# Performance work log

Measured on AMD Instinct MI355X. Metric: run time of the kernel, lower is better.

## Reference

```python
import jax, jax.numpy as jnp
import numpy as np

B, S, N, C, OUT = 16, 1024, 4096, 768, 256


def setup_inputs() -> dict:
    key = jax.random.key(0)
    k0, k1, k2, k3, k4 = jax.random.split(key, 5)
    seed_xyz = jax.random.normal(k0, (B, S, 3), jnp.float32)   # normalized seed coords
    p_last = jax.random.normal(k1, (B, N, 3), jnp.float32)     # lift3d last-stage coords
    f_last = jax.random.normal(k2, (B, C, N), jnp.float32)     # lift3d last-stage features (channel-first)
    W = jax.random.normal(k3, (OUT, C), jnp.float32) * 0.02    # Conv1d(C, 256, kernel_size=1) weight
    b = jax.random.normal(k4, (OUT,), jnp.float32) * 0.02      # Conv1d bias
    return {"seed_xyz": seed_xyz, "p_last": p_last, "f_last": f_last, "W": W, "b": b}


def reference(seed_xyz, p_last, f_last, W, b):
    # Squared pairwise distances [B,S,N] (argmin invariant to sqrt)
    d2 = (jnp.sum(seed_xyz * seed_xyz, axis=-1, keepdims=True)          # [B,S,1]
          - 2.0 * jnp.einsum('bsd,bnd->bsn', seed_xyz, p_last)          # [B,S,N]
          + jnp.sum(p_last * p_last, axis=-1)[:, None, :])              # [B,1,N]
    idx = jnp.argmin(d2, axis=-1)                                       # [B,S]
    # Gather nearest-neighbor features: [B,C,N] -> [B,C,S]
    gathered = jnp.take_along_axis(f_last, idx[:, None, :], axis=2)
    # 1x1 Conv1d projector: [B,C,S] x [OUT,C] -> [B,OUT,S]
    seed_features = jnp.einsum('bcs,oc->bos', gathered, W) + b[None, :, None]
    return seed_features
```

## Files before the change

kernel.cpp:

```cpp
#include <hip/hip_runtime.h>
#include <stdint.h>

#define B_   16
#define S_   1024
#define N_   4096
#define C_   768
#define OUT_ 256

typedef short bf16x8 __attribute__((ext_vector_type(8)));
typedef short bf16x4 __attribute__((ext_vector_type(4)));
typedef float f32x4  __attribute__((ext_vector_type(4)));

__device__ __forceinline__ unsigned short f2bf(float f) {
    unsigned int u = __float_as_uint(f);
    u += 0x7fffu + ((u >> 16) & 1u);
    return (unsigned short)(u >> 16);
}

__global__ __launch_bounds__(256) void k_wconv(const float* __restrict__ W,
                                               unsigned short* __restrict__ Wb) {
    int i = blockIdx.x * 256 + threadIdx.x;
    Wb[i] = f2bf(W[i]);
}

__global__ __launch_bounds__(256) void k_argmin(const float* __restrict__ seed,
                                                const float* __restrict__ pl,
                                                int* __restrict__ idx_out) {
    const int t    = threadIdx.x;
    const int lane = t & 63;
    const int w    = t >> 6;
    const int gw   = blockIdx.x * 4 + w;
    const int b    = gw >> 8;
    const int s0   = (gw & 255) * 4;

    float sx[4], sy[4], sz[4], s2[4], best[4];
    int   bidx[4];
#pragma unroll
    for (int j = 0; j < 4; ++j) {
        const float* sp = seed + (size_t)(b * S_ + s0 + j) * 3;
        sx[j] = sp[0]; sy[j] = sp[1]; sz[j] = sp[2];
        s2[j] = __fadd_rn(__fadd_rn(__fmul_rn(sx[j], sx[j]),
                                    __fmul_rn(sy[j], sy[j])),
                          __fmul_rn(sz[j], sz[j]));
        best[j] = 3.4e38f;
        bidx[j] = 0;
    }
    const float* pb = pl + (size_t)b * N_ * 3;

    for (int k = 0; k < N_ / 64; ++k) {
        const int   n  = k * 64 + lane;
        const float px = pb[n * 3 + 0];
        const float py = pb[n * 3 + 1];
        const float pz = pb[n * 3 + 2];
        const float p2 = __fadd_rn(__fadd_rn(__fmul_rn(px, px),
                                             __fmul_rn(py, py)),
                                   __fmul_rn(pz, pz));
#pragma unroll
        for (int j = 0; j < 4; ++j) {
            float dot = __fadd_rn(__fadd_rn(__fmul_rn(sx[j], px),
                                            __fmul_rn(sy[j], py)),
                                  __fmul_rn(sz[j], pz));
            float d2  = __fadd_rn(__fsub_rn(s2[j], __fmul_rn(2.0f, dot)), p2);
            if (d2 < best[j]) { best[j] = d2; bidx[j] = n; }
        }
    }

#pragma unroll
    for (int j = 0; j < 4; ++j) {
#pragma unroll
        for (int off = 32; off >= 1; off >>= 1) {
            float ob = __shfl_xor(best[j], off, 64);
            int   oi = __shfl_xor(bidx[j], off, 64);
            bool take = (ob < best[j]) || (ob == best[j] && oi < bidx[j]);
            if (take) { best[j] = ob; bidx[j] = oi; }
        }
        if (lane == 0) idx_out[b * S_ + s0 + j] = bidx[j];
    }
}

__global__ __launch_bounds__(256, 2) void k_pgemm(const float* __restrict__ f,
                                                  const unsigned short* __restrict__ Wb,
                                                  unsigned short* __restrict__ P) {
    __shared__ unsigned short ldsF[2][128 * 36];
    __shared__ unsigned short ldsW[2][256 * 40];
    const int t    = threadIdx.x;
    const int b    = blockIdx.x >> 5;
    const int nt   = blockIdx.x & 31;
    const int n0   = nt * 128;
    const int lane = t & 63;
    const int w    = t >> 6;
    const int wm   = w & 1;
    const int wo   = w >> 1;
    const int quad = lane >> 4, l16 = lane & 15;

    f32x4 acc[4][8];
#pragma unroll
    for (int i = 0; i < 4; ++i)
#pragma unroll
        for (int j = 0; j < 8; ++j) acc[i][j] = (f32x4){0.f, 0.f, 0.f, 0.f};

    const int cb = t >> 5;
    const int nb = t & 31;
    const float* fB = f + (size_t)b * C_ * N_ + n0 + nb * 4;
    const int wr = t >> 2;
    const int wc = t & 3;
    const unsigned short* wSrc = Wb + (size_t)wr * C_ + wc * 8;

    f32x4  v[4];
    bf16x8 wv[4];

#pragma unroll
    for (int j = 0; j < 4; ++j)
        v[j] = *(const f32x4*)(fB + (size_t)(cb * 4 + j) * N_);
#pragma unroll
    for (int i = 0; i < 4; ++i)
        wv[i] = *(const bf16x8*)(wSrc + (size_t)i * 64 * C_);
#pragma unroll
    for (int i = 0; i < 4; ++i) {
        bf16x4 pk = {(short)f2bf(v[0][i]), (short)f2bf(v[1][i]),
                     (short)f2bf(v[2][i]), (short)f2bf(v[3][i])};
        *(bf16x4*)(&ldsF[0][(nb * 4 + i) * 36 + cb * 4]) = pk;
    }
#pragma unroll
    for (int i = 0; i < 4; ++i)
        *(bf16x8*)(&ldsW[0][(wr + i * 64) * 40 + wc * 8]) = wv[i];
    __syncthreads();

#pragma unroll 2
    for (int kt = 0; kt < C_ / 32; ++kt) {
        const int rb = kt & 1;
        const unsigned short* fR = &ldsF[rb][0];
        const unsigned short* wR = &ldsW[rb][0];
        unsigned short* fW = &ldsF[rb ^ 1][0];
        unsigned short* wW = &ldsW[rb ^ 1][0];

        if (kt < C_ / 32 - 1) {
            const int k1 = (kt + 1) * 32;
#pragma unroll
            for (int j = 0; j < 4; ++j)
                v[j] = *(const f32x4*)(fB + (size_t)(k1 + cb * 4 + j) * N_);
#pragma unroll
            for (int i = 0; i < 4; ++i)
                wv[i] = *(const bf16x8*)(wSrc + (size_t)i * 64 * C_ + k1);
        }

        bf16x8 aF[4], bF[8];
#pragma unroll
        for (int mi = 0; mi < 4; ++mi) {
            const unsigned short* p = fR + (wm * 64 + mi * 16 + l16) * 36 + quad * 8;
            bf16x4 lo = *(const bf16x4*)p;
            bf16x4 hi = *(const bf16x4*)(p + 4);
            aF[mi] = __builtin_shufflevector(lo, hi, 0, 1, 2, 3, 4, 5, 6, 7);
        }
#pragma unroll
        for (int oi = 0; oi < 8; ++oi)
            bF[oi] = *(const bf16x8*)(wR + (wo * 128 + oi * 16 + l16) * 40 + quad * 8);
#pragma unroll
        for (int mi = 0; mi < 4; ++mi)
#pragma unroll
            for (int oi = 0; oi < 8; ++oi)
                acc[mi][oi] = __builtin_amdgcn_mfma_f32_16x16x32_bf16(
                    aF[mi], bF[oi], acc[mi][oi], 0, 0, 0);

        if (kt < C_ / 32 - 1) {
#pragma unroll
            for (int i = 0; i < 4; ++i) {
                bf16x4 pk = {(short)f2bf(v[0][i]), (short)f2bf(v[1][i]),
                             (short)f2bf(v[2][i]), (short)f2bf(v[3][i])};
                *(bf16x4*)(fW + (nb * 4 + i) * 36 + cb * 4) = pk;
            }
#pragma unroll
            for (int i = 0; i < 4; ++i)
                *(bf16x8*)(wW + (wr + i * 64) * 40 + wc * 8) = wv[i];
        }
        __syncthreads();
    }

    unsigned short* Pb = P + ((size_t)b * N_ + n0) * OUT_;
#pragma unroll
    for (int mi = 0; mi < 4; ++mi) {
#pragma unroll
        for (int r = 0; r < 4; ++r) {
            const int n = wm * 64 + mi * 16 + quad * 4 + r;
            unsigned short* row = Pb + (size_t)n * OUT_;
#pragma unroll
            for (int oi = 0; oi < 8; ++oi) {
                const int o = wo * 128 + oi * 16 + l16;
                row[o] = f2bf(acc[mi][oi][r]);
            }
        }
    }
}

__global__ __launch_bounds__(256) void k_out(const unsigned short* __restrict__ P,
                                             const int* __restrict__ idx,
                                             const float* __restrict__ bias,
                                             float* __restrict__ out) {
    __shared__ unsigned short tl[64 * 260];
    const int t  = threadIdx.x;
    const int b  = blockIdx.x >> 4;
    const int st = blockIdx.x & 15;
    const int s0 = st * 64;
    const unsigned short* Pb = P + (size_t)b * N_ * OUT_;

#pragma unroll
    for (int i = 0; i < 8; ++i) {
        const int g = i * 256 + t;
        const int s = g >> 5;
        const int p = g & 31;
        const int n = idx[b * S_ + s0 + s];
        const unsigned short* src = Pb + (size_t)n * OUT_ + p * 8;
        uint2 u0 = *(const uint2*)src;
        uint2 u1 = *(const uint2*)(src + 4);
        *(uint2*)(tl + s * 260 + p * 8)     = u0;
        *(uint2*)(tl + s * 260 + p * 8 + 4) = u1;
    }
    __syncthreads();

    const int lane = t & 63;
    const int w    = t >> 6;
    float* ob = out + (size_t)b * OUT_ * S_ + s0;
#pragma unroll 4
    for (int oo = 0; oo < 64; ++oo) {
        const int o = w * 64 + oo;
        const unsigned short u = tl[lane * 260 + o];
        const float val = __uint_as_float(((unsigned int)u) << 16) + bias[o];
        ob[(size_t)o * S_ + lane] = val;
    }
}

extern "C" void kernel_launch(void* const* d_in, const int* in_sizes, int n_in,
                              void* d_out, int out_size, void* d_ws, size_t ws_size,
                              hipStream_t stream) {
    const float* seed = (const float*)d_in[0];
    const float* pl   = (const float*)d_in[1];
    const float* f    = (const float*)d_in[2];
    const float* W    = (const float*)d_in[3];
    const float* bias = (const float*)d_in[4];
    float* out = (float*)d_out;

    int* idx            = (int*)d_ws;
    unsigned short* Wb  = (unsigned short*)((char*)d_ws + 65536);
    unsigned short* P   = (unsigned short*)((char*)d_ws + 524288);

    k_wconv <<<768,  256, 0, stream>>>(W, Wb);
    k_argmin<<<1024, 256, 0, stream>>>(seed, pl, idx);
    k_pgemm <<<512,  256, 0, stream>>>(f, Wb, P);
    k_out   <<<256,  256, 0, stream>>>(P, idx, bias, out);
}
```

Baseline: 328.6 us.

## Fuse argmin and projection GEMM into one interleaved launch with deeper prefetch

Merges the nearest-neighbor argmin kernel and the projection GEMM into one launch. One block in three runs a GEMM tile and the other two run argmin, so the compute-bound distance search can overlap the memory-bound feature streaming. The GEMM now prefetches feature rows two k-steps ahead with a double register buffer and uses explicit waitcnt and barrier intrinsics. The weight conversion kernel is also vectorized to eight elements per thread. The risks are higher register pressure in the merged kernel, which could lower occupancy, and load imbalance between the two block types.

```diff
diff --git a/kernel.cpp b/kernel.cpp
--- a/kernel.cpp
+++ b/kernel.cpp
@@ -6,6 +6,7 @@
 #define N_   4096
 #define C_   768
 #define OUT_ 256
+#define NT_  (C_ / 32)
 
 typedef short bf16x8 __attribute__((ext_vector_type(8)));
 typedef short bf16x4 __attribute__((ext_vector_type(4)));
@@ -19,175 +20,191 @@
 
 __global__ __launch_bounds__(256) void k_wconv(const float* __restrict__ W,
                                                unsigned short* __restrict__ Wb) {
-    int i = blockIdx.x * 256 + threadIdx.x;
-    Wb[i] = f2bf(W[i]);
-}
-
-__global__ __launch_bounds__(256) void k_argmin(const float* __restrict__ seed,
-                                                const float* __restrict__ pl,
-                                                int* __restrict__ idx_out) {
-    const int t    = threadIdx.x;
-    const int lane = t & 63;
-    const int w    = t >> 6;
-    const int gw   = blockIdx.x * 4 + w;
-    const int b    = gw >> 8;
-    const int s0   = (gw & 255) * 4;
-
-    float sx[4], sy[4], sz[4], s2[4], best[4];
-    int   bidx[4];
-#pragma unroll
-    for (int j = 0; j < 4; ++j) {
-        const float* sp = seed + (size_t)(b * S_ + s0 + j) * 3;
-        sx[j] = sp[0]; sy[j] = sp[1]; sz[j] = sp[2];
-        s2[j] = __fadd_rn(__fadd_rn(__fmul_rn(sx[j], sx[j]),
-                                    __fmul_rn(sy[j], sy[j])),
-                          __fmul_rn(sz[j], sz[j]));
-        best[j] = 3.4e38f;
-        bidx[j] = 0;
-    }
-    const float* pb = pl + (size_t)b * N_ * 3;
-
-    for (int k = 0; k < N_ / 64; ++k) {
-        const int   n  = k * 64 + lane;
-        const float px = pb[n * 3 + 0];
-        const float py = pb[n * 3 + 1];
-        const float pz = pb[n * 3 + 2];
-        const float p2 = __fadd_rn(__fadd_rn(__fmul_rn(px, px),
-                                             __fmul_rn(py, py)),
-                                   __fmul_rn(pz, pz));
-#pragma unroll
-        for (int j = 0; j < 4; ++j) {
-            float dot = __fadd_rn(__fadd_rn(__fmul_rn(sx[j], px),
-                                            __fmul_rn(sy[j], py)),
-                                  __fmul_rn(sz[j], pz));
-            float d2  = __fadd_rn(__fsub_rn(s2[j], __fmul_rn(2.0f, dot)), p2);
-            if (d2 < best[j]) { best[j] = d2; bidx[j] = n; }
-        }
-    }
-
-#pragma unroll
-    for (int j = 0; j < 4; ++j) {
-#pragma unroll
-        for (int off = 32; off >= 1; off >>= 1) {
-            float ob = __shfl_xor(best[j], off, 64);
-            int   oi = __shfl_xor(bidx[j], off, 64);
-            bool take = (ob < best[j]) || (ob == best[j] && oi < bidx[j]);
-            if (take) { best[j] = ob; bidx[j] = oi; }
-        }
-        if (lane == 0) idx_out[b * S_ + s0 + j] = bidx[j];
-    }
-}
-
-__global__ __launch_bounds__(256, 2) void k_pgemm(const float* __restrict__ f,
+    int i = (blockIdx.x * 256 + threadIdx.x) * 8;
+    f32x4 a = *(const f32x4*)(W + i);
+    f32x4 c = *(const f32x4*)(W + i + 4);
+    bf16x8 o = {(short)f2bf(a[0]), (short)f2bf(a[1]),
+                (short)f2bf(a[2]), (short)f2bf(a[3]),
+                (short)f2bf(c[0]), (short)f2bf(c[1]),
+                (short)f2bf(c[2]), (short)f2bf(c[3])};
+    *(bf16x8*)(Wb + i) = o;
+}
+
+__global__ __launch_bounds__(256, 2) void k_fused(const float* __restrict__ f,
                                                   const unsigned short* __restrict__ Wb,
-                                                  unsigned short* __restrict__ P) {
+                                                  unsigned short* __restrict__ P,
+                                                  const float* __restrict__ seed,
+                                                  const float* __restrict__ pl,
+                                                  int* __restrict__ idx_out) {
     __shared__ unsigned short ldsF[2][128 * 36];
     __shared__ unsigned short ldsW[2][256 * 40];
-    const int t    = threadIdx.x;
-    const int b    = blockIdx.x >> 5;
-    const int nt   = blockIdx.x & 31;
-    const int n0   = nt * 128;
-    const int lane = t & 63;
-    const int w    = t >> 6;
-    const int wm   = w & 1;
-    const int wo   = w >> 1;
-    const int quad = lane >> 4, l16 = lane & 15;
-
-    f32x4 acc[4][8];
-#pragma unroll
-    for (int i = 0; i < 4; ++i)
-#pragma unroll
-        for (int j = 0; j < 8; ++j) acc[i][j] = (f32x4){0.f, 0.f, 0.f, 0.f};
-
-    const int cb = t >> 5;
-    const int nb = t & 31;
-    const float* fB = f + (size_t)b * C_ * N_ + n0 + nb * 4;
-    const int wr = t >> 2;
-    const int wc = t & 3;
-    const unsigned short* wSrc = Wb + (size_t)wr * C_ + wc * 8;
-
-    f32x4  v[4];
-    bf16x8 wv[4];
-
-#pragma unroll
-    for (int j = 0; j < 4; ++j)
-        v[j] = *(const f32x4*)(fB + (size_t)(cb * 4 + j) * N_);
-#pragma unroll
-    for (int i = 0; i < 4; ++i)
-        wv[i] = *(const bf16x8*)(wSrc + (size_t)i * 64 * C_);
-#pragma unroll
-    for (int i = 0; i < 4; ++i) {
-        bf16x4 pk = {(short)f2bf(v[0][i]), (short)f2bf(v[1][i]),
-                     (short)f2bf(v[2][i]), (short)f2bf(v[3][i])};
-        *(bf16x4*)(&ldsF[0][(nb * 4 + i) * 36 + cb * 4]) = pk;
-    }
-#pragma unroll
-    for (int i = 0; i < 4; ++i)
-        *(bf16x8*)(&ldsW[0][(wr + i * 64) * 40 + wc * 8]) = wv[i];
-    __syncthreads();
+    const int bid = blockIdx.x;
+    const int t   = threadIdx.x;
+
+    if (bid % 3 == 0) {
+        const int sub  = bid / 3;
+        const int b    = sub >> 5;
+        const int nt   = sub & 31;
+        const int n0   = nt * 128;
+        const int lane = t & 63;
+        const int w    = t >> 6;
+        const int wm   = w & 1;
+        const int wo   = w >> 1;
+        const int quad = lane >> 4, l16 = lane & 15;
+
+        f32x4 acc[4][8];
+#pragma unroll
+        for (int i = 0; i < 4; ++i)
+#pragma unroll
+            for (int j = 0; j < 8; ++j) acc[i][j] = (f32x4){0.f, 0.f, 0.f, 0.f};
+
+        const int cb = t >> 5;
+        const int nb = t & 31;
+        const float* fB = f + (size_t)b * C_ * N_ + n0 + nb * 4;
+        const int wr = t >> 2;
+        const int wc = t & 3;
+        const unsigned short* wSrc = Wb + (size_t)wr * C_ + wc * 8;
+
+        f32x4  v[2][4];
+        bf16x8 wv[4];
+
+#pragma unroll
+        for (int j = 0; j < 4; ++j)
+            v[0][j] = *(const f32x4*)(fB + (size_t)(cb * 4 + j) * N_);
+#pragma unroll
+        for (int i = 0; i < 4; ++i)
+            wv[i] = *(const bf16x8*)(wSrc + (size_t)i * 64 * C_);
+#pragma unroll
+        for (int i = 0; i < 4; ++i) {
+            bf16x4 pk = {(short)f2bf(v[0][0][i]), (short)f2bf(v[0][1][i]),
+                         (short)f2bf(v[0][2][i]), (short)f2bf(v[0][3][i])};
+            *(bf16x4*)(&ldsF[0][(nb * 4 + i) * 36 + cb * 4]) = pk;
+        }
+#pragma unroll
+        for (int i = 0; i < 4; ++i)
+            *(bf16x8*)(&ldsW[0][(wr + i * 64) * 40 + wc * 8]) = wv[i];
+#pragma unroll
+        for (int j = 0; j < 4; ++j)
+            v[1][j] = *(const f32x4*)(fB + (size_t)(32 + cb * 4 + j) * N_);
+        asm volatile("s_waitcnt lgkmcnt(0)" ::: "memory");
+        __builtin_amdgcn_sched_barrier(0);
+        __builtin_amdgcn_s_barrier();
 
 #pragma unroll 2
-    for (int kt = 0; kt < C_ / 32; ++kt) {
-        const int rb = kt & 1;
-        const unsigned short* fR = &ldsF[rb][0];
-        const unsigned short* wR = &ldsW[rb][0];
-        unsigned short* fW = &ldsF[rb ^ 1][0];
-        unsigned short* wW = &ldsW[rb ^ 1][0];
-
-        if (kt < C_ / 32 - 1) {
-            const int k1 = (kt + 1) * 32;
-#pragma unroll
-            for (int j = 0; j < 4; ++j)
-                v[j] = *(const f32x4*)(fB + (size_t)(k1 + cb * 4 + j) * N_);
-#pragma unroll
-            for (int i = 0; i < 4; ++i)
-                wv[i] = *(const bf16x8*)(wSrc + (size_t)i * 64 * C_ + k1);
-        }
-
-        bf16x8 aF[4], bF[8];
+        for (int kt = 0; kt < NT_; ++kt) {
+            const int rb = kt & 1;
+            if (kt < NT_ - 2) {
+                const int k2 = (kt + 2) * 32;
+#pragma unroll
+                for (int j = 0; j < 4; ++j)
+                    v[rb][j] = *(const f32x4*)(fB + (size_t)(k2 + cb * 4 + j) * N_);
+            }
+            if (kt < NT_ - 1) {
+                const int k1 = (kt + 1) * 32;
+#pragma unroll
+                for (int i = 0; i < 4; ++i)
+                    wv[i] = *(const bf16x8*)(wSrc + (size_t)i * 64 * C_ + k1);
+            }
+
+            bf16x8 aF[4];
+#pragma unroll
+            for (int mi = 0; mi < 4; ++mi) {
+                const unsigned short* p =
+                    &ldsF[rb][(wm * 64 + mi * 16 + l16) * 36 + quad * 8];
+                bf16x4 lo = *(const bf16x4*)p;
+                bf16x4 hi = *(const bf16x4*)(p + 4);
+                aF[mi] = __builtin_shufflevector(lo, hi, 0, 1, 2, 3, 4, 5, 6, 7);
+            }
+#pragma unroll
+            for (int oi = 0; oi < 8; ++oi) {
+                bf16x8 bF = *(const bf16x8*)(
+                    &ldsW[rb][(wo * 128 + oi * 16 + l16) * 40 + quad * 8]);
+#pragma unroll
+                for (int mi = 0; mi < 4; ++mi)
+                    acc[mi][oi] = __builtin_amdgcn_mfma_f32_16x16x32_bf16(
+                        aF[mi], bF, acc[mi][oi], 0, 0, 0);
+            }
+
+            if (kt < NT_ - 1) {
+#pragma unroll
+                for (int i = 0; i < 4; ++i) {
+                    bf16x4 pk = {(short)f2bf(v[rb ^ 1][0][i]), (short)f2bf(v[rb ^ 1][1][i]),
+                                 (short)f2bf(v[rb ^ 1][2][i]), (short)f2bf(v[rb ^ 1][3][i])};
+                    *(bf16x4*)(&ldsF[rb ^ 1][(nb * 4 + i) * 36 + cb * 4]) = pk;
+                }
+#pragma unroll
+                for (int i = 0; i < 4; ++i)
+                    *(bf16x8*)(&ldsW[rb ^ 1][(wr + i * 64) * 40 + wc * 8]) = wv[i];
+            }
+            asm volatile("s_waitcnt lgkmcnt(0)" ::: "memory");
+            __builtin_amdgcn_sched_barrier(0);
+            __builtin_amdgcn_s_barrier();
+        }
+
+        unsigned short* Pb = P + ((size_t)b * N_ + n0) * OUT_;
 #pragma unroll
         for (int mi = 0; mi < 4; ++mi) {
-            const unsigned short* p = fR + (wm * 64 + mi * 16 + l16) * 36 + quad * 8;
-            bf16x4 lo = *(const bf16x4*)p;
-            bf16x4 hi = *(const bf16x4*)(p + 4);
-            aF[mi] = __builtin_shufflevector(lo, hi, 0, 1, 2, 3, 4, 5, 6, 7);
-        }
-#pragma unroll
-        for (int oi = 0; oi < 8; ++oi)
-            bF[oi] = *(const bf16x8*)(wR + (wo * 128 + oi * 16 + l16) * 40 + quad * 8);
-#pragma unroll
-        for (int mi = 0; mi < 4; ++mi)
-#pragma unroll
-            for (int oi = 0; oi < 8; ++oi)
-                acc[mi][oi] = __builtin_amdgcn_mfma_f32_16x16x32_bf16(
-                    aF[mi], bF[oi], acc[mi][oi], 0, 0, 0);
-
-        if (kt < C_ / 32 - 1) {
-#pragma unroll
-            for (int i = 0; i < 4; ++i) {
-                bf16x4 pk = {(short)f2bf(v[0][i]), (short)f2bf(v[1][i]),
-                             (short)f2bf(v[2][i]), (short)f2bf(v[3][i])};
-                *(bf16x4*)(fW + (nb * 4 + i) * 36 + cb * 4) = pk;
-            }
-#pragma unroll
-            for (int i = 0; i < 4; ++i)
-                *(bf16x8*)(wW + (wr + i * 64) * 40 + wc * 8) = wv[i];
-        }
-        __syncthreads();
-    }
-
-    unsigned short* Pb = P + ((size_t)b * N_ + n0) * OUT_;
-#pragma unroll
-    for (int mi = 0; mi < 4; ++mi) {
-#pragma unroll
-        for (int r = 0; r < 4; ++r) {
-            const int n = wm * 64 + mi * 16 + quad * 4 + r;
-            unsigned short* row = Pb + (size_t)n * OUT_;
-#pragma unroll
-            for (int oi = 0; oi < 8; ++oi) {
-                const int o = wo * 128 + oi * 16 + l16;
-                row[o] = f2bf(acc[mi][oi][r]);
-            }
+#pragma unroll
+            for (int r = 0; r < 4; ++r) {
+                const int n = wm * 64 + mi * 16 + quad * 4 + r;
+                unsigned short* row = Pb + (size_t)n * OUT_;
+#pragma unroll
+                for (int oi = 0; oi < 8; ++oi) {
+                    const int o = wo * 128 + oi * 16 + l16;
+                    row[o] = f2bf(acc[mi][oi][r]);
+                }
+            }
+        }
+    } else {
+        const int sub  = bid - bid / 3 - 1;
+        const int lane = t & 63;
+        const int w    = t >> 6;
+        const int gw   = sub * 4 + w;
+        const int b    = gw >> 8;
+        const int s0   = (gw & 255) * 4;
+
+        float sx[4], sy[4], sz[4], s2[4], best[4];
+        int   bidx[4];
+#pragma unroll
+        for (int j = 0; j < 4; ++j) {
+            const float* sp = seed + (size_t)(b * S_ + s0 + j) * 3;
+            sx[j] = sp[0]; sy[j] = sp[1]; sz[j] = sp[2];
+            s2[j] = __fadd_rn(__fadd_rn(__fmul_rn(sx[j], sx[j]),
+                                        __fmul_rn(sy[j], sy[j])),
+                              __fmul_rn(sz[j], sz[j]));
+            best[j] = 3.4e38f;
+            bidx[j] = 0;
+        }
+        const float* pb = pl + (size_t)b * N_ * 3;
+
+        for (int k = 0; k < N_ / 64; ++k) {
+            const int   n  = k * 64 + lane;
+            const float px = pb[n * 3 + 0];
+            const float py = pb[n * 3 + 1];
+            const float pz = pb[n * 3 + 2];
+            const float p2 = __fadd_rn(__fadd_rn(__fmul_rn(px, px),
+                                                 __fmul_rn(py, py)),
+                                       __fmul_rn(pz, pz));
+#pragma unroll
+            for (int j = 0; j < 4; ++j) {
+                float dot = __fadd_rn(__fadd_rn(__fmul_rn(sx[j], px),
+                                                __fmul_rn(sy[j], py)),
+                                      __fmul_rn(sz[j], pz));
+                float d2  = __fadd_rn(__fsub_rn(s2[j], __fmul_rn(2.0f, dot)), p2);
+                if (d2 < best[j]) { best[j] = d2; bidx[j] = n; }
+            }
+        }
+
+#pragma unroll
+        for (int j = 0; j < 4; ++j) {
+#pragma unroll
+            for (int off = 32; off >= 1; off >>= 1) {
+                float ob = __shfl_xor(best[j], off, 64);
+                int   oi = __shfl_xor(bidx[j], off, 64);
+                bool take = (ob < best[j]) || (ob == best[j] && oi < bidx[j]);
+                if (take) { best[j] = ob; bidx[j] = oi; }
+            }
+            if (lane == 0) idx_out[b * S_ + s0 + j] = bidx[j];
         }
     }
 }
@@ -243,8 +260,7 @@
     unsigned short* Wb  = (unsigned short*)((char*)d_ws + 65536);
     unsigned short* P   = (unsigned short*)((char*)d_ws + 524288);
 
-    k_wconv <<<768,  256, 0, stream>>>(W, Wb);
-    k_argmin<<<1024, 256, 0, stream>>>(seed, pl, idx);
-    k_pgemm <<<512,  256, 0, stream>>>(f, Wb, P);
+    k_wconv <<<96,   256, 0, stream>>>(W, Wb);
+    k_fused <<<1536, 256, 0, stream>>>(f, Wb, P, seed, pl, idx);
     k_out   <<<256,  256, 0, stream>>>(P, idx, bias, out);
 }
```

Result: slower. 337.9 us (+2.8%).
